# Kernel tuning notes

Measured on AMD Instinct MI355X. Metric: run time of the kernel, lower is better.

## Reference

```python
import jax, jax.numpy as jnp
import numpy as np

E, H, F = 8, 1024, 4096  # experts, hidden_size, ffn_hidden_size
INIT_STD = 0.02


def setup_inputs() -> dict:
    key = jax.random.key(0)
    kx, k1, k2 = jax.random.split(key, 3)
    total_tokens = 16384
    x = jax.random.normal(kx, (total_tokens, H), dtype=jnp.float32)
    w1 = jax.random.normal(k1, (E, H, F), dtype=jnp.float32) * INIT_STD
    w2 = jax.random.normal(k2, (E, F, H), dtype=jnp.float32) * INIT_STD
    return {"x": x, "w1": w1, "w2": w2, "rows_per_expert": total_tokens // E}


def reference(x, w1, w2, rows_per_expert):
    # Grouped GEMM 1: per-expert x_e @ w1[e]  -> [E, T, F]
    e, h = w1.shape[0], w1.shape[1]
    xg = x.reshape(e, rows_per_expert, h)          # tokens grouped by expert
    inter = jnp.einsum('eth,ehf->etf', xg, w1)     # grouped GEMM 1
    inter = jax.nn.gelu(inter)                     # activation_fn
    out = jnp.einsum('etf,efh->eth', inter, w2)    # grouped GEMM 2
    return out.reshape(-1, h)
```

## Files before the change

kernel.cpp:

```cpp
#include <hip/hip_runtime.h>
#include <hip/hip_bf16.h>


typedef __attribute__((ext_vector_type(8))) short short8;
typedef __attribute__((ext_vector_type(4))) float floatx4;

static __device__ __forceinline__ ushort f2bf(float f) {
  __hip_bfloat16 h = __float2bfloat16(f);
  return *(ushort*)&h;
}


static __device__ __forceinline__ int swz(int n, int o) {
  return o ^ (n & 7) ^ ((n >> 3) & 7);
}

template<int K, int N>
static __device__ __forceinline__ void tpose_tile(const float* __restrict__ in,
                                                  __hip_bfloat16* __restrict__ out,
                                                  ushort* lds, int e, int nt, int kt) {
  const size_t eoff = (size_t)e * K * N;
  const int n0 = nt * 128, k0 = kt * 64;
  const int t = threadIdx.x;
  const int j = t & 15;
  const int g = t >> 4;
  const int o = g >> 1;
  const int h = g & 1;
  const float* src = in + eoff + (size_t)(k0 + 8 * o) * N + n0 + h * 64 + 4 * j;
  float4 v[8];
#pragma unroll
  for (int r = 0; r < 8; ++r)
    v[r] = *(const float4*)(src + (size_t)r * N);
#pragma unroll
  for (int i = 0; i < 4; ++i) {
    const int n = h * 64 + 4 * j + i;
    union { short8 s8; ushort u[8]; } p;
#pragma unroll
    for (int r = 0; r < 8; ++r)
      p.u[r] = f2bf(((const float*)&v[r])[i]);
    *(short8*)(lds + n * 64 + swz(n, o) * 8) = p.s8;
  }
  __syncthreads();
  const int c = t & 7;
  const int r0 = t >> 3;
#pragma unroll
  for (int p = 0; p < 4; ++p) {
    const int n = p * 32 + r0;
    short8 u = *(const short8*)(lds + n * 64 + swz(n, c) * 8);
    *(short8*)(out + eoff + (size_t)(n0 + n) * K + k0 + 8 * c) = u;
  }
}

static __device__ __forceinline__ void cvt_part(const float* __restrict__ x,
                                                __hip_bfloat16* __restrict__ xb, int b) {
  const int t = threadIdx.x;
  const float4* src = (const float4*)x + (size_t)b * 2048 + t;
  ushort4* dst = (ushort4*)xb + (size_t)b * 2048 + t;
#pragma unroll
  for (int u = 0; u < 8; ++u) {
    float4 v = src[u * 256];
    ushort4 q;
    q.x = f2bf(v.x); q.y = f2bf(v.y); q.z = f2bf(v.z); q.w = f2bf(v.w);
    dst[u * 256] = q;
  }
}

__global__ __launch_bounds__(256) void prep(const float* __restrict__ x,
                                            const float* __restrict__ w1,
                                            const float* __restrict__ w2,
                                            __hip_bfloat16* __restrict__ xb,
                                            __hip_bfloat16* __restrict__ w1t,
                                            __hip_bfloat16* __restrict__ w2t) {
  __shared__ __align__(16) ushort lds[128 * 64];
  const int b = blockIdx.x;
  if (b < 2048) {
    cvt_part(x, xb, b);
  } else if (b < 6144) {
    const int bb = b - 2048;
    tpose_tile<1024, 4096>(w1, w1t, lds, bb >> 9, bb & 31, (bb >> 5) & 15);
  } else {
    const int bb = b - 6144;
    tpose_tile<4096, 1024>(w2, w2t, lds, bb >> 9, bb & 7, (bb >> 3) & 63);
  }
}


#define GLDS16(src, dst)                                                       \
  __builtin_amdgcn_global_load_lds(                                            \
      (const __attribute__((address_space(1))) void*)(src),                    \
      (__attribute__((address_space(3))) void*)(dst), 16, 0, 0)

#define WAITVM(n) asm volatile("s_waitcnt vmcnt(" #n ")" ::: "memory")

#define MFMA16(a, b, c) __builtin_amdgcn_mfma_f32_16x16x32_bf16(a, b, c, 0, 0, 0)

static __device__ __forceinline__ void barsync() {
  asm volatile("" ::: "memory");
  __builtin_amdgcn_sched_barrier(0);
  __builtin_amdgcn_s_barrier();
  __builtin_amdgcn_sched_barrier(0);
  asm volatile("" ::: "memory");
}

template<int C>
static __device__ __forceinline__ void ktile(
    int kt, int nt, int t,
    const __hip_bfloat16* __restrict__ aread, const __hip_bfloat16* __restrict__ bread,
    const __hip_bfloat16* __restrict__ Asrc0, const __hip_bfloat16* __restrict__ Asrc1,
    const __hip_bfloat16* __restrict__ Bsrc0, const __hip_bfloat16* __restrict__ Bsrc1,
    __hip_bfloat16* As, __hip_bfloat16* Bs,
    floatx4 (&acc)[8][4]) {
  const int kc1 = (kt + 1) * 64 + 32;
  const int kc2 = (kt + 2) * 64;
  const bool st1 = (kt + 1 < nt);
  const bool st2 = (kt + 2 < nt);
  short8 af[4], bf[4];

#pragma unroll
  for (int i = 0; i < 4; ++i)
    af[i] = *(const short8*)(aread + (C * 2 + 0) * 8192 + i * 512);
#pragma unroll
  for (int j = 0; j < 4; ++j)
    bf[j] = *(const short8*)(bread + (C * 2 + 0) * 8192 + j * 512);
  if (st1) {
    __hip_bfloat16* d = As + ((C ^ 1) * 2 + 1) * 8192;
    GLDS16(Asrc0 + kc1, d + t * 8);
    GLDS16(Asrc1 + kc1, d + 4096 + t * 8);
  }
  barsync();
  __builtin_amdgcn_s_setprio(1);
#pragma unroll
  for (int i = 0; i < 4; ++i)
#pragma unroll
    for (int j = 0; j < 4; ++j)
      acc[i][j] = MFMA16(af[i], bf[j], acc[i][j]);
  __builtin_amdgcn_s_setprio(0);
  barsync();

#pragma unroll
  for (int i = 0; i < 4; ++i)
    af[i] = *(const short8*)(aread + (C * 2 + 0) * 8192 + 2048 + i * 512);
  if (st1) {
    __hip_bfloat16* d = Bs + ((C ^ 1) * 2 + 1) * 8192;
    GLDS16(Bsrc0 + kc1, d + t * 8);
    GLDS16(Bsrc1 + kc1, d + 4096 + t * 8);
  }
  barsync();
  __builtin_amdgcn_s_setprio(1);
#pragma unroll
  for (int i = 0; i < 4; ++i)
#pragma unroll
    for (int j = 0; j < 4; ++j)
      acc[i + 4][j] = MFMA16(af[i], bf[j], acc[i + 4][j]);
  __builtin_amdgcn_s_setprio(0);
  barsync();

#pragma unroll
  for (int i = 0; i < 4; ++i)
    af[i] = *(const short8*)(aread + (C * 2 + 1) * 8192 + i * 512);
#pragma unroll
  for (int j = 0; j < 4; ++j)
    bf[j] = *(const short8*)(bread + (C * 2 + 1) * 8192 + j * 512);
  if (st2) {
    __hip_bfloat16* d = As + (C * 2 + 0) * 8192;
    GLDS16(Asrc0 + kc2, d + t * 8);
    GLDS16(Asrc1 + kc2, d + 4096 + t * 8);
  }
  barsync();
  __builtin_amdgcn_s_setprio(1);
#pragma unroll
  for (int i = 0; i < 4; ++i)
#pragma unroll
    for (int j = 0; j < 4; ++j)
      acc[i][j] = MFMA16(af[i], bf[j], acc[i][j]);
  __builtin_amdgcn_s_setprio(0);
  barsync();

#pragma unroll
  for (int i = 0; i < 4; ++i)
    af[i] = *(const short8*)(aread + (C * 2 + 1) * 8192 + 2048 + i * 512);
  if (st2) {
    __hip_bfloat16* d = Bs + (C * 2 + 0) * 8192;
    GLDS16(Bsrc0 + kc2, d + t * 8);
    GLDS16(Bsrc1 + kc2, d + 4096 + t * 8);
  }
  barsync();
  __builtin_amdgcn_s_setprio(1);
#pragma unroll
  for (int i = 0; i < 4; ++i)
#pragma unroll
    for (int j = 0; j < 4; ++j)
      acc[i + 4][j] = MFMA16(af[i], bf[j], acc[i + 4][j]);
  __builtin_amdgcn_s_setprio(0);
  if (st2) { WAITVM(4); } else { WAITVM(0); }
  barsync();
}

template<bool GELU, typename OutT>
__global__ __launch_bounds__(512, 2) void gemm8(
    const __hip_bfloat16* __restrict__ A, const __hip_bfloat16* __restrict__ Bt,
    OutT* __restrict__ C, int M, int N, int K) {
  __shared__ __align__(16) __hip_bfloat16 lds[65536];
  __hip_bfloat16* As = lds;
  __hip_bfloat16* Bs = lds + 32768;

  const int e = blockIdx.z;
  A  += (size_t)e * M * K;
  Bt += (size_t)e * N * K;
  C  += (size_t)e * M * N;

  const int MT = M >> 8, NT = N >> 8;
  const int lin = blockIdx.x;
  const int xcd = lin & 7;
  const int idx = lin >> 3;
  const int mh = MT >> 1, nq = NT >> 2;
  const int mt  = (xcd >> 2) * mh + idx % mh;
  const int nti = (xcd & 3) * nq + idx / mh;
  const int m0 = mt << 8, n0 = nti << 8;

  const int t = threadIdx.x;
  const int lane = t & 63;
  const int l16 = lane & 15;
  const int quad = lane >> 4;
  const int w = t >> 6;
  const int wr = w >> 2;
  const int wc = w & 3;
  const int sx = (quad ^ ((l16 >> 1) & 3)) * 8;

  const __hip_bfloat16* aread = As + (wr * 128 + l16) * 32 + sx;
  const __hip_bfloat16* bread = Bs + (wc * 64 + l16) * 32 + sx;

  const int r0s = t >> 2;
  const int q0s = ((t & 3) ^ ((r0s >> 1) & 3)) * 8;
  const int r1s = r0s + 128;
  const int q1s = ((t & 3) ^ ((r1s >> 1) & 3)) * 8;
  const __hip_bfloat16* Asrc0 = A  + (size_t)(m0 + r0s) * K + q0s;
  const __hip_bfloat16* Asrc1 = A  + (size_t)(m0 + r1s) * K + q1s;
  const __hip_bfloat16* Bsrc0 = Bt + (size_t)(n0 + r0s) * K + q0s;
  const __hip_bfloat16* Bsrc1 = Bt + (size_t)(n0 + r1s) * K + q1s;

  const int nt = K >> 6;
  floatx4 acc[8][4] = {};

  GLDS16(Asrc0 + 0,  As + t * 8);            GLDS16(Asrc1 + 0,  As + 4096 + t * 8);
  GLDS16(Bsrc0 + 0,  Bs + t * 8);            GLDS16(Bsrc1 + 0,  Bs + 4096 + t * 8);
  GLDS16(Asrc0 + 32, As + 8192 + t * 8);     GLDS16(Asrc1 + 32, As + 12288 + t * 8);
  GLDS16(Bsrc0 + 32, Bs + 8192 + t * 8);     GLDS16(Bsrc1 + 32, Bs + 12288 + t * 8);
  if (nt > 1) {
    GLDS16(Asrc0 + 64, As + 16384 + t * 8);  GLDS16(Asrc1 + 64, As + 20480 + t * 8);
    GLDS16(Bsrc0 + 64, Bs + 16384 + t * 8);  GLDS16(Bsrc1 + 64, Bs + 20480 + t * 8);
    WAITVM(4);
  } else {
    WAITVM(0);
  }
  barsync();

  for (int kt = 0; kt < nt; kt += 2) {
    ktile<0>(kt,     nt, t, aread, bread, Asrc0, Asrc1, Bsrc0, Bsrc1, As, Bs, acc);
    ktile<1>(kt + 1, nt, t, aread, bread, Asrc0, Asrc1, Bsrc0, Bsrc1, As, Bs, acc);
  }

  const int mrow = m0 + wr * 128 + quad * 4;
  const int ncol = n0 + wc * 64 + l16;
#pragma unroll
  for (int i = 0; i < 8; ++i) {
#pragma unroll
    for (int r = 0; r < 4; ++r) {
      OutT* crow = C + (size_t)(mrow + i * 16 + r) * N + ncol;
#pragma unroll
      for (int j = 0; j < 4; ++j) {
        float v = acc[i][j][r];
        if constexpr (GELU) {
          const float u2 = 1.5957691216057308f * (v + 0.044715f * v * v * v);
          const float ex = __expf(u2);
          v = v - v * __builtin_amdgcn_rcpf(ex + 1.0f);
        }
        if constexpr (sizeof(OutT) == 2)
          crow[j * 16] = __float2bfloat16(v);
        else
          crow[j * 16] = v;
      }
    }
  }
}

extern "C" void kernel_launch(void* const* d_in, const int* in_sizes, int n_in,
                              void* d_out, int out_size, void* d_ws, size_t ws_size,
                              hipStream_t stream) {
  const float* x  = (const float*)d_in[0];
  const float* w1 = (const float*)d_in[1];
  const float* w2 = (const float*)d_in[2];
  float* out = (float*)d_out;

  char* ws = (char*)d_ws;
  __hip_bfloat16* xb    = (__hip_bfloat16*)(ws);
  __hip_bfloat16* w1t   = (__hip_bfloat16*)(ws + (size_t)32 * 1024 * 1024);
  __hip_bfloat16* w2t   = (__hip_bfloat16*)(ws + (size_t)96 * 1024 * 1024);
  __hip_bfloat16* inter = (__hip_bfloat16*)(ws + (size_t)160 * 1024 * 1024);

  prep<<<10240, 256, 0, stream>>>(x, w1, w2, xb, w1t, w2t);
  gemm8<true, __hip_bfloat16>
      <<<dim3(128, 1, 8), 512, 0, stream>>>(xb, w1t, inter, 2048, 4096, 1024);
  gemm8<false, float>
      <<<dim3(32, 1, 8), 512, 0, stream>>>(inter, w2t, out, 2048, 1024, 4096);
}
```

Measured before the change: 619.6 us.

## Merge half-tile phases in k-tile loop to halve barrier count

Restructures the k-tile body from four half-phases, each with two barriers, into two phases. Each phase issues both A and B global-to-LDS prefetches up front, loads all eight A fragments at once, and runs 32 MFMAs between barriers. The goal is to cut barrier synchronisation overhead and give the MFMA stream longer uninterrupted runs. The cost is more VGPR pressure from holding eight A fragments, which could hurt occupancy at the two-blocks-per-SM launch bound. It also drops the barrier between the LDS fragment reads and the MFMAs, so correctness relies on the existing wait/barrier ordering.

```diff
diff --git a/kernel.cpp b/kernel.cpp
--- a/kernel.cpp
+++ b/kernel.cpp
@@ -114,83 +114,53 @@
   const int kc2 = (kt + 2) * 64;
   const bool st1 = (kt + 1 < nt);
   const bool st2 = (kt + 2 < nt);
-  short8 af[4], bf[4];
-
-#pragma unroll
-  for (int i = 0; i < 4; ++i)
+  short8 af[8], bf[4];
+
+  if (st1) {
+    __hip_bfloat16* dA = As + ((C ^ 1) * 2 + 1) * 8192;
+    GLDS16(Asrc0 + kc1, dA + t * 8);
+    GLDS16(Asrc1 + kc1, dA + 4096 + t * 8);
+    __hip_bfloat16* dB = Bs + ((C ^ 1) * 2 + 1) * 8192;
+    GLDS16(Bsrc0 + kc1, dB + t * 8);
+    GLDS16(Bsrc1 + kc1, dB + 4096 + t * 8);
+  }
+#pragma unroll
+  for (int i = 0; i < 8; ++i)
     af[i] = *(const short8*)(aread + (C * 2 + 0) * 8192 + i * 512);
 #pragma unroll
   for (int j = 0; j < 4; ++j)
     bf[j] = *(const short8*)(bread + (C * 2 + 0) * 8192 + j * 512);
-  if (st1) {
-    __hip_bfloat16* d = As + ((C ^ 1) * 2 + 1) * 8192;
-    GLDS16(Asrc0 + kc1, d + t * 8);
-    GLDS16(Asrc1 + kc1, d + 4096 + t * 8);
-  }
-  barsync();
+  __builtin_amdgcn_sched_barrier(0);
   __builtin_amdgcn_s_setprio(1);
 #pragma unroll
-  for (int i = 0; i < 4; ++i)
+  for (int i = 0; i < 8; ++i)
 #pragma unroll
     for (int j = 0; j < 4; ++j)
       acc[i][j] = MFMA16(af[i], bf[j], acc[i][j]);
   __builtin_amdgcn_s_setprio(0);
   barsync();
 
-#pragma unroll
-  for (int i = 0; i < 4; ++i)
-    af[i] = *(const short8*)(aread + (C * 2 + 0) * 8192 + 2048 + i * 512);
-  if (st1) {
-    __hip_bfloat16* d = Bs + ((C ^ 1) * 2 + 1) * 8192;
-    GLDS16(Bsrc0 + kc1, d + t * 8);
-    GLDS16(Bsrc1 + kc1, d + 4096 + t * 8);
-  }
-  barsync();
-  __builtin_amdgcn_s_setprio(1);
-#pragma unroll
-  for (int i = 0; i < 4; ++i)
-#pragma unroll
-    for (int j = 0; j < 4; ++j)
-      acc[i + 4][j] = MFMA16(af[i], bf[j], acc[i + 4][j]);
-  __builtin_amdgcn_s_setprio(0);
-  barsync();
-
-#pragma unroll
-  for (int i = 0; i < 4; ++i)
+  if (st2) {
+    __hip_bfloat16* dA = As + (C * 2 + 0) * 8192;
+    GLDS16(Asrc0 + kc2, dA + t * 8);
+    GLDS16(Asrc1 + kc2, dA + 4096 + t * 8);
+    __hip_bfloat16* dB = Bs + (C * 2 + 0) * 8192;
+    GLDS16(Bsrc0 + kc2, dB + t * 8);
+    GLDS16(Bsrc1 + kc2, dB + 4096 + t * 8);
+  }
+#pragma unroll
+  for (int i = 0; i < 8; ++i)
     af[i] = *(const short8*)(aread + (C * 2 + 1) * 8192 + i * 512);
 #pragma unroll
   for (int j = 0; j < 4; ++j)
     bf[j] = *(const short8*)(bread + (C * 2 + 1) * 8192 + j * 512);
-  if (st2) {
-    __hip_bfloat16* d = As + (C * 2 + 0) * 8192;
-    GLDS16(Asrc0 + kc2, d + t * 8);
-    GLDS16(Asrc1 + kc2, d + 4096 + t * 8);
-  }
-  barsync();
+  __builtin_amdgcn_sched_barrier(0);
   __builtin_amdgcn_s_setprio(1);
 #pragma unroll
-  for (int i = 0; i < 4; ++i)
+  for (int i = 0; i < 8; ++i)
 #pragma unroll
     for (int j = 0; j < 4; ++j)
       acc[i][j] = MFMA16(af[i], bf[j], acc[i][j]);
-  __builtin_amdgcn_s_setprio(0);
-  barsync();
-
-#pragma unroll
-  for (int i = 0; i < 4; ++i)
-    af[i] = *(const short8*)(aread + (C * 2 + 1) * 8192 + 2048 + i * 512);
-  if (st2) {
-    __hip_bfloat16* d = Bs + (C * 2 + 0) * 8192;
-    GLDS16(Bsrc0 + kc2, d + t * 8);
-    GLDS16(Bsrc1 + kc2, d + 4096 + t * 8);
-  }
-  barsync();
-  __builtin_amdgcn_s_setprio(1);
-#pragma unroll
-  for (int i = 0; i < 4; ++i)
-#pragma unroll
-    for (int j = 0; j < 4; ++j)
-      acc[i + 4][j] = MFMA16(af[i], bf[j], acc[i + 4][j]);
   __builtin_amdgcn_s_setprio(0);
   if (st2) { WAITVM(4); } else { WAITVM(0); }
   barsync();
```

New measurement: 623.6 us. Within noise of the previous version (+0.6%).
